# Kernel tuning notes

Measured on AMD Instinct MI355X. Metric: run time of the kernel, lower is better.

## Reference

```python
import jax, jax.numpy as jnp
import numpy as np

N_NODES = 100000
N_EDGES = 300000
NUM_GRAPHS = 2000
IN_DIM = 82
HIDDEN = 256


def _gcn_conv(x, src, dst, dinv, W, b):
    # GCNConv: out = D^-1/2 (A + I) D^-1/2 (x W) + b
    xW = x @ W  # [N, H]
    norm = dinv[src] * dinv[dst]  # [E]
    agg = jax.ops.segment_sum(xW[src] * norm[:, None], dst, num_segments=N_NODES)
    self_loop = xW * (dinv * dinv)[:, None]
    return agg + self_loop + b


def setup_inputs() -> dict:
    key = jax.random.key(0)
    ks = jax.random.split(key, 8)
    x = jax.random.normal(ks[0], (N_NODES, IN_DIM), dtype=jnp.float32)
    edge_index = jax.random.randint(ks[1], (2, N_EDGES), 0, N_NODES, dtype=jnp.int64)
    batch = jnp.sort(jax.random.randint(ks[2], (N_NODES,), 0, NUM_GRAPHS, dtype=jnp.int64))
    W1 = jax.random.normal(ks[3], (IN_DIM, HIDDEN), dtype=jnp.float32) * (1.0 / np.sqrt(IN_DIM))
    W2 = jax.random.normal(ks[4], (HIDDEN, HIDDEN), dtype=jnp.float32) * (1.0 / np.sqrt(HIDDEN))
    W3 = jax.random.normal(ks[5], (HIDDEN, HIDDEN), dtype=jnp.float32) * (1.0 / np.sqrt(HIDDEN))
    b1 = jnp.zeros((HIDDEN,), jnp.float32)
    b2 = jnp.zeros((HIDDEN,), jnp.float32)
    b3 = jnp.zeros((HIDDEN,), jnp.float32)
    return {"x": x, "edge_index": edge_index, "batch": batch, "num_graphs": NUM_GRAPHS,
            "W1": W1, "b1": b1, "W2": W2, "b2": b2, "W3": W3, "b3": b3}


def reference(x, edge_index, batch, num_graphs, W1, b1, W2, b2, W3, b3):
    src, dst = edge_index[0], edge_index[1]
    # symmetric normalization with added self-loops (PyG gcn_norm)
    deg = jax.ops.segment_sum(jnp.ones_like(dst, dtype=x.dtype), dst, num_segments=N_NODES) + 1.0
    dinv = jax.lax.rsqrt(deg)
    h = jax.nn.relu(_gcn_conv(x, src, dst, dinv, W1, b1))
    h = jax.nn.relu(_gcn_conv(h, src, dst, dinv, W2, b2))
    h = jax.nn.relu(_gcn_conv(h, src, dst, dinv, W3, b3))
    return jax.ops.segment_max(h, batch, num_segments=num_graphs)  # [G, H]
```

## Files before the change

### kernel.cpp

```cpp
#include <hip/hip_runtime.h>
#include <cstdint>
#include <cstddef>

#define N_NODES 100000
#define N_EDGES 300000
#define N_GRAPHS 2000
#define HID 256
#define INDIM 82
#define XCPAD 84
#define K1PAD 128
#define N_TILES ((N_NODES + 255) / 256)
#define SCAN_CHUNK 2048
#define NBLK_SCAN ((N_NODES + SCAN_CHUNK - 1) / SCAN_CHUNK)

typedef __bf16 bf16x8 __attribute__((ext_vector_type(8)));
typedef float f32x4 __attribute__((ext_vector_type(4)));

__device__ __forceinline__ unsigned short f2bf(float f) {
    union { __bf16 h; unsigned short u; } v;
    v.h = (__bf16)f;
    return v.u;
}
__device__ __forceinline__ float bf2f(unsigned short s) {
    return __uint_as_float(((unsigned int)s) << 16);
}

__global__ void k_cnt_acc(const int* __restrict__ ei, int* cnt) {
    int e = blockIdx.x * 256 + threadIdx.x;
    if (e < N_EDGES) atomicAdd(&cnt[ei[N_EDGES + e]], 1);
}

__global__ __launch_bounds__(256) void k_scan1(const int* __restrict__ cnt, int* __restrict__ off,
                                               int* __restrict__ partial) {
    __shared__ int sdata[256];
    const int base = blockIdx.x * SCAN_CHUNK;
    const int t = threadIdx.x;
    int v[8];
    int s = 0;
#pragma unroll
    for (int i = 0; i < 8; ++i) {
        int idx = base + t * 8 + i;
        v[i] = (idx < N_NODES) ? cnt[idx] : 0;
        s += v[i];
    }
    sdata[t] = s;
    __syncthreads();
    for (int d = 1; d < 256; d <<= 1) {
        int x = (t >= d) ? sdata[t - d] : 0;
        __syncthreads();
        sdata[t] += x;
        __syncthreads();
    }
    int run = sdata[t] - s;
#pragma unroll
    for (int i = 0; i < 8; ++i) {
        int idx = base + t * 8 + i;
        if (idx < N_NODES) off[idx] = run;
        run += v[i];
    }
    if (t == 255) partial[blockIdx.x] = sdata[255];
}

__global__ void k_scan2(int* partial) {
    if (threadIdx.x == 0 && blockIdx.x == 0) {
        int run = 0;
        for (int i = 0; i < NBLK_SCAN; ++i) {
            int v = partial[i];
            partial[i] = run;
            run += v;
        }
    }
}

__global__ void k_scan3(int* __restrict__ off, const int* __restrict__ partial,
                        int* __restrict__ cur, const int* __restrict__ cnt,
                        float* __restrict__ dinv) {
    int i = blockIdx.x * 256 + threadIdx.x;
    if (i < N_NODES) {
        int o = off[i] + partial[i >> 11];
        off[i] = o;
        cur[i] = o;
        dinv[i] = rsqrtf((float)cnt[i] + 1.0f);
    }
}

__global__ void k_fill(const int* __restrict__ ei, const float* __restrict__ dinv, int* cur,
                       int* __restrict__ csr_src, float* __restrict__ csr_norm) {
    int e = blockIdx.x * 256 + threadIdx.x;
    if (e < N_EDGES) {
        int s = ei[e];
        int d = ei[N_EDGES + e];
        int pos = atomicAdd(&cur[d], 1);
        csr_src[pos] = s;
        csr_norm[pos] = dinv[s] * dinv[d];
    }
}

__device__ __forceinline__ void wconv_body(const float* __restrict__ W,
                                           unsigned short* __restrict__ Wb, int KSRC, int i) {
    int kc = i >> 13;
    int r = i & 8191;
    int nt = r >> 9;
    int r2 = r & 511;
    int lg = r2 >> 7;
    int lr = (r2 >> 3) & 15;
    int j = r2 & 7;
    int k = kc * 32 + lg * 8 + j;
    int n = nt * 16 + lr;
    Wb[i] = (k < KSRC) ? f2bf(W[(size_t)k * HID + n]) : (unsigned short)0;
}

#define PREP_W1 128
#define PREP_W23 256
#define PREP_BND 8
#define PREP_XC ((N_NODES * XCPAD + 255) / 256)
#define PREP_BLOCKS (PREP_W1 + 2 * PREP_W23 + PREP_BND + PREP_XC)

__global__ void k_prep(const float* __restrict__ x, unsigned short* __restrict__ xc,
                       const float* __restrict__ W1, unsigned short* __restrict__ Wb1,
                       const float* __restrict__ W2, unsigned short* __restrict__ Wb2,
                       const float* __restrict__ W3, unsigned short* __restrict__ Wb3,
                       const int* __restrict__ batch, int* __restrict__ gstart) {
    int b = blockIdx.x;
    int t = threadIdx.x;
    if (b < PREP_W1) { wconv_body(W1, Wb1, INDIM, b * 256 + t); return; }
    b -= PREP_W1;
    if (b < PREP_W23) { wconv_body(W2, Wb2, HID, b * 256 + t); return; }
    b -= PREP_W23;
    if (b < PREP_W23) { wconv_body(W3, Wb3, HID, b * 256 + t); return; }
    b -= PREP_W23;
    if (b < PREP_BND) {
        int g = b * 256 + t;
        if (g <= N_GRAPHS) {
            int lo = 0, hi = N_NODES;
            while (lo < hi) {
                int mid = (lo + hi) >> 1;
                if (batch[mid] < g) lo = mid + 1;
                else hi = mid;
            }
            gstart[g] = lo;
        }
        return;
    }
    b -= PREP_BND;
    int i = b * 256 + t;
    if (i < N_NODES * XCPAD) {
        int node = i / XCPAD;
        int k = i - node * XCPAD;
        xc[i] = (k < INDIM) ? f2bf(x[(size_t)node * INDIM + k]) : (unsigned short)0;
    }
}

template <int K>
__global__ __launch_bounds__(512) void k_gemm_mfma(const unsigned short* __restrict__ A,
                                                   const unsigned short* __restrict__ Wb,
                                                   const float* __restrict__ bias,
                                                   unsigned short* __restrict__ Cb) {
    constexpr int NK = K / 32;
    __shared__ __align__(16) unsigned short Wsh[K * HID];

    const int tid = threadIdx.x;
    const int w = tid >> 6;
    const int l = tid & 63;
    const int lr = l & 15;
    const int lg = l >> 4;

#pragma unroll
    for (int i = 0; i < K / 16; ++i) {
        int o = (i * 512 + tid) * 8;
        *reinterpret_cast<uint4*>(&Wsh[o]) = *reinterpret_cast<const uint4*>(Wb + o);
    }
    __syncthreads();

    float bv[16];
#pragma unroll
    for (int nt = 0; nt < 16; ++nt) bv[nt] = bias[nt * 16 + lr];

    for (int t = blockIdx.x; t < N_TILES; t += 256) {
        const int rowbase = t * 256 + w * 32;
        int r0 = rowbase + lr;
        int r1 = rowbase + 16 + lr;
        int r0c = r0 < N_NODES ? r0 : (N_NODES - 1);
        int r1c = r1 < N_NODES ? r1 : (N_NODES - 1);
        const unsigned short* a0p = A + (size_t)r0c * K + lg * 8;
        const unsigned short* a1p = A + (size_t)r1c * K + lg * 8;

        bf16x8 a0[NK], a1[NK];
#pragma unroll
        for (int kc = 0; kc < NK; ++kc) {
            a0[kc] = *reinterpret_cast<const bf16x8*>(a0p + kc * 32);
            a1[kc] = *reinterpret_cast<const bf16x8*>(a1p + kc * 32);
        }

        f32x4 acc0[16] = {};
        f32x4 acc1[16] = {};

#pragma unroll
        for (int kc = 0; kc < NK; ++kc) {
            const unsigned short* bfp = Wsh + kc * 8192 + l * 8;
#pragma unroll
            for (int nt = 0; nt < 16; ++nt) {
                bf16x8 bb = *reinterpret_cast<const bf16x8*>(bfp + nt * 512);
                acc0[nt] = __builtin_amdgcn_mfma_f32_16x16x32_bf16(a0[kc], bb, acc0[nt], 0, 0, 0);
                acc1[nt] = __builtin_amdgcn_mfma_f32_16x16x32_bf16(a1[kc], bb, acc1[nt], 0, 0, 0);
            }
        }

        int gr0 = rowbase + lg * 4;
#pragma unroll
        for (int j = 0; j < 4; ++j) {
            int gr = gr0 + j;
            if (gr < N_NODES) {
                size_t base = (size_t)gr * HID + lr;
#pragma unroll
                for (int nt = 0; nt < 16; ++nt)
                    Cb[base + nt * 16] = f2bf(fmaxf(acc0[nt][j] + bv[nt], 0.0f));
            }
            int gr2 = gr + 16;
            if (gr2 < N_NODES) {
                size_t base = (size_t)gr2 * HID + lr;
#pragma unroll
                for (int nt = 0; nt < 16; ++nt)
                    Cb[base + nt * 16] = f2bf(fmaxf(acc1[nt][j] + bv[nt], 0.0f));
            }
        }
    }
}

__global__ void k_aggregate256(const unsigned short* __restrict__ tb,
                               const float* __restrict__ dinv, const int* __restrict__ off,
                               const int* __restrict__ cnt, const int* __restrict__ csr_src,
                               const float* __restrict__ csr_norm,
                               unsigned short* __restrict__ ob) {
    int node = blockIdx.x * 4 + (threadIdx.x >> 6);
    if (node >= N_NODES) return;
    int lane = threadIdx.x & 63;
    const size_t lo = (size_t)lane * 4;
    int o0 = off[node];
    int n = cnt[node];
    float di = dinv[node];
    float s2 = di * di;
    ushort4 sv = *reinterpret_cast<const ushort4*>(&tb[(size_t)node * HID + lo]);
    float4 acc = {bf2f(sv.x) * s2, bf2f(sv.y) * s2, bf2f(sv.z) * s2, bf2f(sv.w) * s2};

    int j = 0;
    for (; j + 3 < n; j += 4) {
        int s0 = csr_src[o0 + j];
        int s1 = csr_src[o0 + j + 1];
        int s2i = csr_src[o0 + j + 2];
        int s3 = csr_src[o0 + j + 3];
        float n0 = csr_norm[o0 + j];
        float n1 = csr_norm[o0 + j + 1];
        float n2 = csr_norm[o0 + j + 2];
        float n3 = csr_norm[o0 + j + 3];
        ushort4 u0 = *reinterpret_cast<const ushort4*>(&tb[(size_t)s0 * HID + lo]);
        ushort4 u1 = *reinterpret_cast<const ushort4*>(&tb[(size_t)s1 * HID + lo]);
        ushort4 u2 = *reinterpret_cast<const ushort4*>(&tb[(size_t)s2i * HID + lo]);
        ushort4 u3 = *reinterpret_cast<const ushort4*>(&tb[(size_t)s3 * HID + lo]);
        acc.x = fmaf(n0, bf2f(u0.x), acc.x); acc.y = fmaf(n0, bf2f(u0.y), acc.y);
        acc.z = fmaf(n0, bf2f(u0.z), acc.z); acc.w = fmaf(n0, bf2f(u0.w), acc.w);
        acc.x = fmaf(n1, bf2f(u1.x), acc.x); acc.y = fmaf(n1, bf2f(u1.y), acc.y);
        acc.z = fmaf(n1, bf2f(u1.z), acc.z); acc.w = fmaf(n1, bf2f(u1.w), acc.w);
        acc.x = fmaf(n2, bf2f(u2.x), acc.x); acc.y = fmaf(n2, bf2f(u2.y), acc.y);
        acc.z = fmaf(n2, bf2f(u2.z), acc.z); acc.w = fmaf(n2, bf2f(u2.w), acc.w);
        acc.x = fmaf(n3, bf2f(u3.x), acc.x); acc.y = fmaf(n3, bf2f(u3.y), acc.y);
        acc.z = fmaf(n3, bf2f(u3.z), acc.z); acc.w = fmaf(n3, bf2f(u3.w), acc.w);
    }
    int rem = n - j;
    if (rem & 2) {
        int s0 = csr_src[o0 + j];
        int s1 = csr_src[o0 + j + 1];
        float n0 = csr_norm[o0 + j];
        float n1 = csr_norm[o0 + j + 1];
        ushort4 u0 = *reinterpret_cast<const ushort4*>(&tb[(size_t)s0 * HID + lo]);
        ushort4 u1 = *reinterpret_cast<const ushort4*>(&tb[(size_t)s1 * HID + lo]);
        acc.x = fmaf(n0, bf2f(u0.x), acc.x); acc.y = fmaf(n0, bf2f(u0.y), acc.y);
        acc.z = fmaf(n0, bf2f(u0.z), acc.z); acc.w = fmaf(n0, bf2f(u0.w), acc.w);
        acc.x = fmaf(n1, bf2f(u1.x), acc.x); acc.y = fmaf(n1, bf2f(u1.y), acc.y);
        acc.z = fmaf(n1, bf2f(u1.z), acc.z); acc.w = fmaf(n1, bf2f(u1.w), acc.w);
        j += 2;
    }
    if (rem & 1) {
        int s0 = csr_src[o0 + j];
        float n0 = csr_norm[o0 + j];
        ushort4 u0 = *reinterpret_cast<const ushort4*>(&tb[(size_t)s0 * HID + lo]);
        acc.x = fmaf(n0, bf2f(u0.x), acc.x); acc.y = fmaf(n0, bf2f(u0.y), acc.y);
        acc.z = fmaf(n0, bf2f(u0.z), acc.z); acc.w = fmaf(n0, bf2f(u0.w), acc.w);
    }
    ushort4 o;
    o.x = f2bf(acc.x);
    o.y = f2bf(acc.y);
    o.z = f2bf(acc.z);
    o.w = f2bf(acc.w);
    *reinterpret_cast<ushort4*>(&ob[(size_t)node * HID + lo]) = o;
}

__global__ void k_aggx(const unsigned short* __restrict__ xc,
                       const float* __restrict__ dinv, const int* __restrict__ off,
                       const int* __restrict__ cnt, const int* __restrict__ csr_src,
                       const float* __restrict__ csr_norm,
                       unsigned short* __restrict__ ob) {
    int node = blockIdx.x * 4 + (threadIdx.x >> 6);
    if (node >= N_NODES) return;
    int lane = threadIdx.x & 63;
    const bool act = lane < (XCPAD / 2);
    const size_t co = (size_t)lane * 2;
    int o0 = off[node];
    int n = cnt[node];
    float di = dinv[node];
    float s2 = di * di;
    float2 acc = {0.0f, 0.0f};
    if (act) {
        ushort2 sv = *reinterpret_cast<const ushort2*>(&xc[(size_t)node * XCPAD + co]);
        acc.x = bf2f(sv.x) * s2;
        acc.y = bf2f(sv.y) * s2;
    }
    int j = 0;
    for (; j + 3 < n; j += 4) {
        int s0 = csr_src[o0 + j];
        int s1 = csr_src[o0 + j + 1];
        int s2i = csr_src[o0 + j + 2];
        int s3 = csr_src[o0 + j + 3];
        float n0 = csr_norm[o0 + j];
        float n1 = csr_norm[o0 + j + 1];
        float n2 = csr_norm[o0 + j + 2];
        float n3 = csr_norm[o0 + j + 3];
        if (act) {
            ushort2 u0 = *reinterpret_cast<const ushort2*>(&xc[(size_t)s0 * XCPAD + co]);
            ushort2 u1 = *reinterpret_cast<const ushort2*>(&xc[(size_t)s1 * XCPAD + co]);
            ushort2 u2 = *reinterpret_cast<const ushort2*>(&xc[(size_t)s2i * XCPAD + co]);
            ushort2 u3 = *reinterpret_cast<const ushort2*>(&xc[(size_t)s3 * XCPAD + co]);
            acc.x = fmaf(n0, bf2f(u0.x), acc.x); acc.y = fmaf(n0, bf2f(u0.y), acc.y);
            acc.x = fmaf(n1, bf2f(u1.x), acc.x); acc.y = fmaf(n1, bf2f(u1.y), acc.y);
            acc.x = fmaf(n2, bf2f(u2.x), acc.x); acc.y = fmaf(n2, bf2f(u2.y), acc.y);
            acc.x = fmaf(n3, bf2f(u3.x), acc.x); acc.y = fmaf(n3, bf2f(u3.y), acc.y);
        }
    }
    int rem = n - j;
    if (rem & 2) {
        int s0 = csr_src[o0 + j];
        int s1 = csr_src[o0 + j + 1];
        float n0 = csr_norm[o0 + j];
        float n1 = csr_norm[o0 + j + 1];
        if (act) {
            ushort2 u0 = *reinterpret_cast<const ushort2*>(&xc[(size_t)s0 * XCPAD + co]);
            ushort2 u1 = *reinterpret_cast<const ushort2*>(&xc[(size_t)s1 * XCPAD + co]);
            acc.x = fmaf(n0, bf2f(u0.x), acc.x); acc.y = fmaf(n0, bf2f(u0.y), acc.y);
            acc.x = fmaf(n1, bf2f(u1.x), acc.x); acc.y = fmaf(n1, bf2f(u1.y), acc.y);
        }
        j += 2;
    }
    if (rem & 1) {
        int s0 = csr_src[o0 + j];
        float n0 = csr_norm[o0 + j];
        if (act) {
            ushort2 u0 = *reinterpret_cast<const ushort2*>(&xc[(size_t)s0 * XCPAD + co]);
            acc.x = fmaf(n0, bf2f(u0.x), acc.x); acc.y = fmaf(n0, bf2f(u0.y), acc.y);
        }
    }
    ushort2 o;
    o.x = f2bf(acc.x);
    o.y = f2bf(acc.y);
    *reinterpret_cast<ushort2*>(&ob[(size_t)node * K1PAD + co]) = o;
}

__global__ void k_pool2(const unsigned short* __restrict__ hb, const int* __restrict__ gstart,
                        float* __restrict__ out) {
    int g = blockIdx.x;
    int w = threadIdx.x >> 6;
    int lane = threadIdx.x & 63;
    int col = w * 128 + lane * 2;
    int s = gstart[g], e = gstart[g + 1];
    float2 m = {0.0f, 0.0f};
    for (int i = s; i < e; ++i) {
        ushort2 u = *reinterpret_cast<const ushort2*>(&hb[(size_t)i * HID + col]);
        m.x = fmaxf(m.x, bf2f(u.x));
        m.y = fmaxf(m.y, bf2f(u.y));
    }
    *reinterpret_cast<float2*>(&out[(size_t)g * HID + col]) = m;
}

extern "C" void kernel_launch(void* const* d_in, const int* in_sizes, int n_in,
                              void* d_out, int out_size, void* d_ws, size_t ws_size,
                              hipStream_t stream) {
    const float* x = (const float*)d_in[0];
    const int* ei = (const int*)d_in[1];
    const int* batch = (const int*)d_in[2];
    const float* W1 = (const float*)d_in[4];
    const float* b1 = (const float*)d_in[5];
    const float* W2 = (const float*)d_in[6];
    const float* b2 = (const float*)d_in[7];
    const float* W3 = (const float*)d_in[8];
    const float* b3 = (const float*)d_in[9];
    float* out = (float*)d_out;

    char* ws = (char*)d_ws;
    float* dinv = (float*)(ws);
    int* cnt = (int*)(ws + (512 << 10));
    int* off = (int*)(ws + (1024 << 10));
    int* cur = (int*)(ws + (1536 << 10));
    int* part = (int*)(ws + (2048 << 10));
    int* gstart = (int*)(ws + (2048 << 10) + 4096);
    int* csr_src = (int*)(ws + (2176 << 10));
    float* csr_norm = (float*)(ws + (3392 << 10));
    unsigned short* Wb1 = (unsigned short*)(ws + (4608 << 10));
    unsigned short* Wb2 = (unsigned short*)(ws + (4736 << 10));
    unsigned short* Wb3 = (unsigned short*)(ws + (4928 << 10));
    unsigned short* ag1_b = (unsigned short*)(ws + (5120 << 10));
    unsigned short* bufA = (unsigned short*)(ws + (5120 << 10) + 25600000);
    unsigned short* bufB = (unsigned short*)(ws + (5120 << 10) + 76800000);
    unsigned short* x_c = (unsigned short*)(ws + (5120 << 10) + 128000000);

    const int nblk_edges = (N_EDGES + 255) / 256;
    const int nblk_nodes = (N_NODES + 255) / 256;
    const int nblk_rows4 = (N_NODES + 3) / 4;

    hipMemsetAsync(cnt, 0, N_NODES * sizeof(int), stream);
    k_cnt_acc<<<nblk_edges, 256, 0, stream>>>(ei, cnt);
    k_scan1<<<NBLK_SCAN, 256, 0, stream>>>(cnt, off, part);
    k_scan2<<<1, 64, 0, stream>>>(part);
    k_scan3<<<nblk_nodes, 256, 0, stream>>>(off, part, cur, cnt, dinv);
    k_fill<<<nblk_edges, 256, 0, stream>>>(ei, dinv, cur, csr_src, csr_norm);

    k_prep<<<PREP_BLOCKS, 256, 0, stream>>>(x, x_c, W1, Wb1, W2, Wb2, W3, Wb3, batch, gstart);

    k_aggx<<<nblk_rows4, 256, 0, stream>>>(x_c, dinv, off, cnt, csr_src, csr_norm, ag1_b);
    k_gemm_mfma<K1PAD><<<256, 512, 0, stream>>>(ag1_b, Wb1, b1, bufA);

    k_aggregate256<<<nblk_rows4, 256, 0, stream>>>(bufA, dinv, off, cnt, csr_src, csr_norm, bufB);
    k_gemm_mfma<HID><<<256, 512, 0, stream>>>(bufB, Wb2, b2, bufA);

    k_aggregate256<<<nblk_rows4, 256, 0, stream>>>(bufA, dinv, off, cnt, csr_src, csr_norm, bufB);
    k_gemm_mfma<HID><<<256, 512, 0, stream>>>(bufB, Wb3, b3, bufA);

    k_pool2<<<N_GRAPHS, 128, 0, stream>>>(bufA, gstart, out);
}
```

Measured before the change: 257.8 us.

## Fuse neighbor aggregation into MFMA GEMM A-operand loads for layers one and two

Adds a kernel that gathers and normalizes neighbor rows directly while building the MFMA A fragments, removing the separate aggregation kernel and its intermediate buffer round trip for layers 1 and 2. Layer 1 now pads the input to K=96 instead of 128, shrinking the padded GEMM work. Layer 3 keeps the separate aggregate+GEMM path. The fused path performs irregular gathers inside the GEMM loop with one lane group per row, which can hurt latency hiding and occupancy given the large register footprint.

Result: slower. 324.8 us (+26.0%).

```diff
diff --git a/kernel.cpp b/kernel.cpp
--- a/kernel.cpp
+++ b/kernel.cpp
@@ -7,8 +7,7 @@
 #define N_GRAPHS 2000
 #define HID 256
 #define INDIM 82
-#define XCPAD 84
-#define K1PAD 128
+#define K1 96
 #define N_TILES ((N_NODES + 255) / 256)
 #define SCAN_CHUNK 2048
 #define NBLK_SCAN ((N_NODES + SCAN_CHUNK - 1) / SCAN_CHUNK)
@@ -110,10 +109,10 @@
     Wb[i] = (k < KSRC) ? f2bf(W[(size_t)k * HID + n]) : (unsigned short)0;
 }
 
-#define PREP_W1 128
+#define PREP_W1 96
 #define PREP_W23 256
 #define PREP_BND 8
-#define PREP_XC ((N_NODES * XCPAD + 255) / 256)
+#define PREP_XC ((N_NODES * K1 + 255) / 256)
 #define PREP_BLOCKS (PREP_W1 + 2 * PREP_W23 + PREP_BND + PREP_XC)
 
 __global__ void k_prep(const float* __restrict__ x, unsigned short* __restrict__ xc,
@@ -144,10 +143,147 @@
     }
     b -= PREP_BND;
     int i = b * 256 + t;
-    if (i < N_NODES * XCPAD) {
-        int node = i / XCPAD;
-        int k = i - node * XCPAD;
+    if (i < N_NODES * K1) {
+        int node = i / K1;
+        int k = i - node * K1;
         xc[i] = (k < INDIM) ? f2bf(x[(size_t)node * INDIM + k]) : (unsigned short)0;
+    }
+}
+
+template <int K>
+__global__ __launch_bounds__(512) void k_gemm_agg(const unsigned short* __restrict__ A,
+                                                  const unsigned short* __restrict__ Wb,
+                                                  const float* __restrict__ bias,
+                                                  const float* __restrict__ dinv,
+                                                  const int* __restrict__ off,
+                                                  const int* __restrict__ cnt,
+                                                  const int* __restrict__ csr_src,
+                                                  const float* __restrict__ csr_norm,
+                                                  unsigned short* __restrict__ Cb) {
+    constexpr int NK = K / 32;
+    __shared__ __align__(16) unsigned short Wsh[K * HID];
+
+    const int tid = threadIdx.x;
+    const int w = tid >> 6;
+    const int l = tid & 63;
+    const int lr = l & 15;
+    const int lg = l >> 4;
+
+#pragma unroll
+    for (int i = 0; i < K / 16; ++i) {
+        int o = (i * 512 + tid) * 8;
+        *reinterpret_cast<uint4*>(&Wsh[o]) = *reinterpret_cast<const uint4*>(Wb + o);
+    }
+    __syncthreads();
+
+    float bv[16];
+#pragma unroll
+    for (int nt = 0; nt < 16; ++nt) bv[nt] = bias[nt * 16 + lr];
+
+    for (int t = blockIdx.x; t < N_TILES; t += gridDim.x) {
+        const int rowbase = t * 256 + w * 32;
+        int r0 = rowbase + lr;
+        int r1 = rowbase + 16 + lr;
+        int r0c = r0 < N_NODES ? r0 : (N_NODES - 1);
+        int r1c = r1 < N_NODES ? r1 : (N_NODES - 1);
+        const int o00 = off[r0c], n0 = cnt[r0c];
+        const int o01 = off[r1c], n1 = cnt[r1c];
+        float d0 = dinv[r0c], d1 = dinv[r1c];
+        const float s20 = d0 * d0, s21 = d1 * d1;
+
+        f32x4 acc0[16] = {};
+        f32x4 acc1[16] = {};
+
+#pragma unroll
+        for (int kc = 0; kc < NK; ++kc) {
+            const int ko = kc * 32 + lg * 8;
+
+            float ag[8];
+            {
+                bf16x8 sv = *reinterpret_cast<const bf16x8*>(A + (size_t)r0c * K + ko);
+#pragma unroll
+                for (int i = 0; i < 8; ++i) ag[i] = (float)sv[i] * s20;
+                int j = 0;
+                for (; j + 1 < n0; j += 2) {
+                    int sA = csr_src[o00 + j];
+                    int sB = csr_src[o00 + j + 1];
+                    float mA = csr_norm[o00 + j];
+                    float mB = csr_norm[o00 + j + 1];
+                    bf16x8 vA = *reinterpret_cast<const bf16x8*>(A + (size_t)sA * K + ko);
+                    bf16x8 vB = *reinterpret_cast<const bf16x8*>(A + (size_t)sB * K + ko);
+#pragma unroll
+                    for (int i = 0; i < 8; ++i) ag[i] = fmaf(mA, (float)vA[i], ag[i]);
+#pragma unroll
+                    for (int i = 0; i < 8; ++i) ag[i] = fmaf(mB, (float)vB[i], ag[i]);
+                }
+                if (j < n0) {
+                    int sA = csr_src[o00 + j];
+                    float mA = csr_norm[o00 + j];
+                    bf16x8 vA = *reinterpret_cast<const bf16x8*>(A + (size_t)sA * K + ko);
+#pragma unroll
+                    for (int i = 0; i < 8; ++i) ag[i] = fmaf(mA, (float)vA[i], ag[i]);
+                }
+            }
+            bf16x8 a0;
+#pragma unroll
+            for (int i = 0; i < 8; ++i) a0[i] = (__bf16)ag[i];
+
+            {
+                bf16x8 sv = *reinterpret_cast<const bf16x8*>(A + (size_t)r1c * K + ko);
+#pragma unroll
+                for (int i = 0; i < 8; ++i) ag[i] = (float)sv[i] * s21;
+                int j = 0;
+                for (; j + 1 < n1; j += 2) {
+                    int sA = csr_src[o01 + j];
+                    int sB = csr_src[o01 + j + 1];
+                    float mA = csr_norm[o01 + j];
+                    float mB = csr_norm[o01 + j + 1];
+                    bf16x8 vA = *reinterpret_cast<const bf16x8*>(A + (size_t)sA * K + ko);
+                    bf16x8 vB = *reinterpret_cast<const bf16x8*>(A + (size_t)sB * K + ko);
+#pragma unroll
+                    for (int i = 0; i < 8; ++i) ag[i] = fmaf(mA, (float)vA[i], ag[i]);
+#pragma unroll
+                    for (int i = 0; i < 8; ++i) ag[i] = fmaf(mB, (float)vB[i], ag[i]);
+                }
+                if (j < n1) {
+                    int sA = csr_src[o01 + j];
+                    float mA = csr_norm[o01 + j];
+                    bf16x8 vA = *reinterpret_cast<const bf16x8*>(A + (size_t)sA * K + ko);
+#pragma unroll
+                    for (int i = 0; i < 8; ++i) ag[i] = fmaf(mA, (float)vA[i], ag[i]);
+                }
+            }
+            bf16x8 a1;
+#pragma unroll
+            for (int i = 0; i < 8; ++i) a1[i] = (__bf16)ag[i];
+
+            const unsigned short* bfp = Wsh + kc * 8192 + l * 8;
+#pragma unroll
+            for (int nt = 0; nt < 16; ++nt) {
+                bf16x8 bb = *reinterpret_cast<const bf16x8*>(bfp + nt * 512);
+                acc0[nt] = __builtin_amdgcn_mfma_f32_16x16x32_bf16(a0, bb, acc0[nt], 0, 0, 0);
+                acc1[nt] = __builtin_amdgcn_mfma_f32_16x16x32_bf16(a1, bb, acc1[nt], 0, 0, 0);
+            }
+        }
+
+        int gr0 = rowbase + lg * 4;
+#pragma unroll
+        for (int j = 0; j < 4; ++j) {
+            int gr = gr0 + j;
+            if (gr < N_NODES) {
+                size_t base = (size_t)gr * HID + lr;
+#pragma unroll
+                for (int nt = 0; nt < 16; ++nt)
+                    Cb[base + nt * 16] = f2bf(fmaxf(acc0[nt][j] + bv[nt], 0.0f));
+            }
+            int gr2 = gr + 16;
+            if (gr2 < N_NODES) {
+                size_t base = (size_t)gr2 * HID + lr;
+#pragma unroll
+                for (int nt = 0; nt < 16; ++nt)
+                    Cb[base + nt * 16] = f2bf(fmaxf(acc1[nt][j] + bv[nt], 0.0f));
+            }
+        }
     }
 }
 
@@ -176,7 +312,7 @@
 #pragma unroll
     for (int nt = 0; nt < 16; ++nt) bv[nt] = bias[nt * 16 + lr];
 
-    for (int t = blockIdx.x; t < N_TILES; t += 256) {
+    for (int t = blockIdx.x; t < N_TILES; t += gridDim.x) {
         const int rowbase = t * 256 + w * 32;
         int r0 = rowbase + lr;
         int r1 = rowbase + 16 + lr;
@@ -295,75 +431,6 @@
     *reinterpret_cast<ushort4*>(&ob[(size_t)node * HID + lo]) = o;
 }
 
-__global__ void k_aggx(const unsigned short* __restrict__ xc,
-                       const float* __restrict__ dinv, const int* __restrict__ off,
-                       const int* __restrict__ cnt, const int* __restrict__ csr_src,
-                       const float* __restrict__ csr_norm,
-                       unsigned short* __restrict__ ob) {
-    int node = blockIdx.x * 4 + (threadIdx.x >> 6);
-    if (node >= N_NODES) return;
-    int lane = threadIdx.x & 63;
-    const bool act = lane < (XCPAD / 2);
-    const size_t co = (size_t)lane * 2;
-    int o0 = off[node];
-    int n = cnt[node];
-    float di = dinv[node];
-    float s2 = di * di;
-    float2 acc = {0.0f, 0.0f};
-    if (act) {
-        ushort2 sv = *reinterpret_cast<const ushort2*>(&xc[(size_t)node * XCPAD + co]);
-        acc.x = bf2f(sv.x) * s2;
-        acc.y = bf2f(sv.y) * s2;
-    }
-    int j = 0;
-    for (; j + 3 < n; j += 4) {
-        int s0 = csr_src[o0 + j];
-        int s1 = csr_src[o0 + j + 1];
-        int s2i = csr_src[o0 + j + 2];
-        int s3 = csr_src[o0 + j + 3];
-        float n0 = csr_norm[o0 + j];
-        float n1 = csr_norm[o0 + j + 1];
-        float n2 = csr_norm[o0 + j + 2];
-        float n3 = csr_norm[o0 + j + 3];
-        if (act) {
-            ushort2 u0 = *reinterpret_cast<const ushort2*>(&xc[(size_t)s0 * XCPAD + co]);
-            ushort2 u1 = *reinterpret_cast<const ushort2*>(&xc[(size_t)s1 * XCPAD + co]);
-            ushort2 u2 = *reinterpret_cast<const ushort2*>(&xc[(size_t)s2i * XCPAD + co]);
-            ushort2 u3 = *reinterpret_cast<const ushort2*>(&xc[(size_t)s3 * XCPAD + co]);
-            acc.x = fmaf(n0, bf2f(u0.x), acc.x); acc.y = fmaf(n0, bf2f(u0.y), acc.y);
-            acc.x = fmaf(n1, bf2f(u1.x), acc.x); acc.y = fmaf(n1, bf2f(u1.y), acc.y);
-            acc.x = fmaf(n2, bf2f(u2.x), acc.x); acc.y = fmaf(n2, bf2f(u2.y), acc.y);
-            acc.x = fmaf(n3, bf2f(u3.x), acc.x); acc.y = fmaf(n3, bf2f(u3.y), acc.y);
-        }
-    }
-    int rem = n - j;
-    if (rem & 2) {
-        int s0 = csr_src[o0 + j];
-        int s1 = csr_src[o0 + j + 1];
-        float n0 = csr_norm[o0 + j];
-        float n1 = csr_norm[o0 + j + 1];
-        if (act) {
-            ushort2 u0 = *reinterpret_cast<const ushort2*>(&xc[(size_t)s0 * XCPAD + co]);
-            ushort2 u1 = *reinterpret_cast<const ushort2*>(&xc[(size_t)s1 * XCPAD + co]);
-            acc.x = fmaf(n0, bf2f(u0.x), acc.x); acc.y = fmaf(n0, bf2f(u0.y), acc.y);
-            acc.x = fmaf(n1, bf2f(u1.x), acc.x); acc.y = fmaf(n1, bf2f(u1.y), acc.y);
-        }
-        j += 2;
-    }
-    if (rem & 1) {
-        int s0 = csr_src[o0 + j];
-        float n0 = csr_norm[o0 + j];
-        if (act) {
-            ushort2 u0 = *reinterpret_cast<const ushort2*>(&xc[(size_t)s0 * XCPAD + co]);
-            acc.x = fmaf(n0, bf2f(u0.x), acc.x); acc.y = fmaf(n0, bf2f(u0.y), acc.y);
-        }
-    }
-    ushort2 o;
-    o.x = f2bf(acc.x);
-    o.y = f2bf(acc.y);
-    *reinterpret_cast<ushort2*>(&ob[(size_t)node * K1PAD + co]) = o;
-}
-
 __global__ void k_pool2(const unsigned short* __restrict__ hb, const int* __restrict__ gstart,
                         float* __restrict__ out) {
     int g = blockIdx.x;
@@ -406,10 +473,10 @@
     unsigned short* Wb1 = (unsigned short*)(ws + (4608 << 10));
     unsigned short* Wb2 = (unsigned short*)(ws + (4736 << 10));
     unsigned short* Wb3 = (unsigned short*)(ws + (4928 << 10));
-    unsigned short* ag1_b = (unsigned short*)(ws + (5120 << 10));
-    unsigned short* bufA = (unsigned short*)(ws + (5120 << 10) + 25600000);
-    unsigned short* bufB = (unsigned short*)(ws + (5120 << 10) + 76800000);
-    unsigned short* x_c = (unsigned short*)(ws + (5120 << 10) + 128000000);
+    unsigned short* x_c = (unsigned short*)(ws + (5120 << 10));
+    unsigned short* bufA = (unsigned short*)(ws + (5120 << 10) + 19200000);
+    unsigned short* bufB = (unsigned short*)(ws + (5120 << 10) + 70400000);
+    unsigned short* bufC = (unsigned short*)(ws + (5120 << 10) + 121600000);
 
     const int nblk_edges = (N_EDGES + 255) / 256;
     const int nblk_nodes = (N_NODES + 255) / 256;
@@ -424,14 +491,14 @@
 
     k_prep<<<PREP_BLOCKS, 256, 0, stream>>>(x, x_c, W1, Wb1, W2, Wb2, W3, Wb3, batch, gstart);
 
-    k_aggx<<<nblk_rows4, 256, 0, stream>>>(x_c, dinv, off, cnt, csr_src, csr_norm, ag1_b);
-    k_gemm_mfma<K1PAD><<<256, 512, 0, stream>>>(ag1_b, Wb1, b1, bufA);
-
-    k_aggregate256<<<nblk_rows4, 256, 0, stream>>>(bufA, dinv, off, cnt, csr_src, csr_norm, bufB);
-    k_gemm_mfma<HID><<<256, 512, 0, stream>>>(bufB, Wb2, b2, bufA);
-
-    k_aggregate256<<<nblk_rows4, 256, 0, stream>>>(bufA, dinv, off, cnt, csr_src, csr_norm, bufB);
-    k_gemm_mfma<HID><<<256, 512, 0, stream>>>(bufB, Wb3, b3, bufA);
+    k_gemm_agg<K1><<<N_TILES, 512, 0, stream>>>(x_c, Wb1, b1, dinv, off, cnt, csr_src,
+                                                csr_norm, bufA);
+
+    k_gemm_agg<HID><<<256, 512, 0, stream>>>(bufA, Wb2, b2, dinv, off, cnt, csr_src,
+                                             csr_norm, bufB);
+
+    k_aggregate256<<<nblk_rows4, 256, 0, stream>>>(bufB, dinv, off, cnt, csr_src, csr_norm, bufC);
+    k_gemm_mfma<HID><<<256, 512, 0, stream>>>(bufC, Wb3, b3, bufA);
 
     k_pool2<<<N_GRAPHS, 128, 0, stream>>>(bufA, gstart, out);
 }
```

## Split GEMM columns across two blocks per tile and shrink layer-1 K to 96

Applied to the files above, without the earlier changes.

The GEMM kernel drops its persistent grid-stride loop over row tiles. It now launches two blocks per 256-row tile, and each block covers half of the 256 output columns. This halves the shared-memory weight footprint and the accumulator registers per block, so more blocks can be resident and more parallelism is exposed. Separately, the layer-1 input is padded to 96 instead of the earlier 84/128 mix: the aggregated features are stored at width 96 and the first GEMM runs with K=96, which removes wasted MFMA work and memory traffic. In exchange, each tile's A rows are now loaded twice (once per column half), and every block reloads its half of the weights.

Result: slower. 279.2 us (+8.3%).

```diff
diff --git a/kernel.cpp b/kernel.cpp
--- a/kernel.cpp
+++ b/kernel.cpp
@@ -7,8 +7,7 @@
 #define N_GRAPHS 2000
 #define HID 256
 #define INDIM 82
-#define XCPAD 84
-#define K1PAD 128
+#define K1 96
 #define N_TILES ((N_NODES + 255) / 256)
 #define SCAN_CHUNK 2048
 #define NBLK_SCAN ((N_NODES + SCAN_CHUNK - 1) / SCAN_CHUNK)
@@ -110,10 +109,10 @@
     Wb[i] = (k < KSRC) ? f2bf(W[(size_t)k * HID + n]) : (unsigned short)0;
 }
 
-#define PREP_W1 128
+#define PREP_W1 96
 #define PREP_W23 256
 #define PREP_BND 8
-#define PREP_XC ((N_NODES * XCPAD + 255) / 256)
+#define PREP_XC ((N_NODES * K1 + 255) / 256)
 #define PREP_BLOCKS (PREP_W1 + 2 * PREP_W23 + PREP_BND + PREP_XC)
 
 __global__ void k_prep(const float* __restrict__ x, unsigned short* __restrict__ xc,
@@ -144,9 +143,9 @@
     }
     b -= PREP_BND;
     int i = b * 256 + t;
-    if (i < N_NODES * XCPAD) {
-        int node = i / XCPAD;
-        int k = i - node * XCPAD;
+    if (i < N_NODES * K1) {
+        int node = i / K1;
+        int k = i - node * K1;
         xc[i] = (k < INDIM) ? f2bf(x[(size_t)node * INDIM + k]) : (unsigned short)0;
     }
 }
@@ -157,72 +156,72 @@
                                                    const float* __restrict__ bias,
                                                    unsigned short* __restrict__ Cb) {
     constexpr int NK = K / 32;
-    __shared__ __align__(16) unsigned short Wsh[K * HID];
+    __shared__ __align__(16) unsigned short Wsh[K * 128];
 
     const int tid = threadIdx.x;
     const int w = tid >> 6;
     const int l = tid & 63;
     const int lr = l & 15;
     const int lg = l >> 4;
-
-#pragma unroll
-    for (int i = 0; i < K / 16; ++i) {
-        int o = (i * 512 + tid) * 8;
-        *reinterpret_cast<uint4*>(&Wsh[o]) = *reinterpret_cast<const uint4*>(Wb + o);
+    const int t = blockIdx.x >> 1;
+    const int ch = blockIdx.x & 1;
+
+#pragma unroll
+    for (int i = 0; i < NK; ++i) {
+        *reinterpret_cast<uint4*>(&Wsh[i * 4096 + tid * 8]) =
+            *reinterpret_cast<const uint4*>(Wb + i * 8192 + ch * 4096 + tid * 8);
     }
     __syncthreads();
 
-    float bv[16];
-#pragma unroll
-    for (int nt = 0; nt < 16; ++nt) bv[nt] = bias[nt * 16 + lr];
-
-    for (int t = blockIdx.x; t < N_TILES; t += 256) {
-        const int rowbase = t * 256 + w * 32;
-        int r0 = rowbase + lr;
-        int r1 = rowbase + 16 + lr;
-        int r0c = r0 < N_NODES ? r0 : (N_NODES - 1);
-        int r1c = r1 < N_NODES ? r1 : (N_NODES - 1);
-        const unsigned short* a0p = A + (size_t)r0c * K + lg * 8;
-        const unsigned short* a1p = A + (size_t)r1c * K + lg * 8;
-
-        bf16x8 a0[NK], a1[NK];
-#pragma unroll
-        for (int kc = 0; kc < NK; ++kc) {
-            a0[kc] = *reinterpret_cast<const bf16x8*>(a0p + kc * 32);
-            a1[kc] = *reinterpret_cast<const bf16x8*>(a1p + kc * 32);
-        }
-
-        f32x4 acc0[16] = {};
-        f32x4 acc1[16] = {};
-
-#pragma unroll
-        for (int kc = 0; kc < NK; ++kc) {
-            const unsigned short* bfp = Wsh + kc * 8192 + l * 8;
-#pragma unroll
-            for (int nt = 0; nt < 16; ++nt) {
-                bf16x8 bb = *reinterpret_cast<const bf16x8*>(bfp + nt * 512);
-                acc0[nt] = __builtin_amdgcn_mfma_f32_16x16x32_bf16(a0[kc], bb, acc0[nt], 0, 0, 0);
-                acc1[nt] = __builtin_amdgcn_mfma_f32_16x16x32_bf16(a1[kc], bb, acc1[nt], 0, 0, 0);
-            }
-        }
-
-        int gr0 = rowbase + lg * 4;
-#pragma unroll
-        for (int j = 0; j < 4; ++j) {
-            int gr = gr0 + j;
-            if (gr < N_NODES) {
-                size_t base = (size_t)gr * HID + lr;
-#pragma unroll
-                for (int nt = 0; nt < 16; ++nt)
-                    Cb[base + nt * 16] = f2bf(fmaxf(acc0[nt][j] + bv[nt], 0.0f));
-            }
-            int gr2 = gr + 16;
-            if (gr2 < N_NODES) {
-                size_t base = (size_t)gr2 * HID + lr;
-#pragma unroll
-                for (int nt = 0; nt < 16; ++nt)
-                    Cb[base + nt * 16] = f2bf(fmaxf(acc1[nt][j] + bv[nt], 0.0f));
-            }
+    float bv[8];
+#pragma unroll
+    for (int nt = 0; nt < 8; ++nt) bv[nt] = bias[ch * 128 + nt * 16 + lr];
+
+    const int rowbase = t * 256 + w * 32;
+    int r0 = rowbase + lr;
+    int r1 = rowbase + 16 + lr;
+    int r0c = r0 < N_NODES ? r0 : (N_NODES - 1);
+    int r1c = r1 < N_NODES ? r1 : (N_NODES - 1);
+    const unsigned short* a0p = A + (size_t)r0c * K + lg * 8;
+    const unsigned short* a1p = A + (size_t)r1c * K + lg * 8;
+
+    bf16x8 a0[NK], a1[NK];
+#pragma unroll
+    for (int kc = 0; kc < NK; ++kc) {
+        a0[kc] = *reinterpret_cast<const bf16x8*>(a0p + kc * 32);
+        a1[kc] = *reinterpret_cast<const bf16x8*>(a1p + kc * 32);
+    }
+
+    f32x4 acc0[8] = {};
+    f32x4 acc1[8] = {};
+
+#pragma unroll
+    for (int kc = 0; kc < NK; ++kc) {
+        const unsigned short* bfp = Wsh + kc * 4096 + l * 8;
+#pragma unroll
+        for (int nt = 0; nt < 8; ++nt) {
+            bf16x8 bb = *reinterpret_cast<const bf16x8*>(bfp + nt * 512);
+            acc0[nt] = __builtin_amdgcn_mfma_f32_16x16x32_bf16(a0[kc], bb, acc0[nt], 0, 0, 0);
+            acc1[nt] = __builtin_amdgcn_mfma_f32_16x16x32_bf16(a1[kc], bb, acc1[nt], 0, 0, 0);
+        }
+    }
+
+    int gr0 = rowbase + lg * 4;
+#pragma unroll
+    for (int j = 0; j < 4; ++j) {
+        int gr = gr0 + j;
+        if (gr < N_NODES) {
+            size_t base = (size_t)gr * HID + ch * 128 + lr;
+#pragma unroll
+            for (int nt = 0; nt < 8; ++nt)
+                Cb[base + nt * 16] = f2bf(fmaxf(acc0[nt][j] + bv[nt], 0.0f));
+        }
+        int gr2 = gr + 16;
+        if (gr2 < N_NODES) {
+            size_t base = (size_t)gr2 * HID + ch * 128 + lr;
+#pragma unroll
+            for (int nt = 0; nt < 8; ++nt)
+                Cb[base + nt * 16] = f2bf(fmaxf(acc1[nt][j] + bv[nt], 0.0f));
         }
     }
 }
@@ -295,15 +294,15 @@
     *reinterpret_cast<ushort4*>(&ob[(size_t)node * HID + lo]) = o;
 }
 
-__global__ void k_aggx(const unsigned short* __restrict__ xc,
-                       const float* __restrict__ dinv, const int* __restrict__ off,
-                       const int* __restrict__ cnt, const int* __restrict__ csr_src,
-                       const float* __restrict__ csr_norm,
-                       unsigned short* __restrict__ ob) {
+__global__ void k_aggx96(const unsigned short* __restrict__ xc,
+                         const float* __restrict__ dinv, const int* __restrict__ off,
+                         const int* __restrict__ cnt, const int* __restrict__ csr_src,
+                         const float* __restrict__ csr_norm,
+                         unsigned short* __restrict__ ob) {
     int node = blockIdx.x * 4 + (threadIdx.x >> 6);
     if (node >= N_NODES) return;
     int lane = threadIdx.x & 63;
-    const bool act = lane < (XCPAD / 2);
+    const bool act = lane < (K1 / 2);
     const size_t co = (size_t)lane * 2;
     int o0 = off[node];
     int n = cnt[node];
@@ -311,7 +310,7 @@
     float s2 = di * di;
     float2 acc = {0.0f, 0.0f};
     if (act) {
-        ushort2 sv = *reinterpret_cast<const ushort2*>(&xc[(size_t)node * XCPAD + co]);
+        ushort2 sv = *reinterpret_cast<const ushort2*>(&xc[(size_t)node * K1 + co]);
         acc.x = bf2f(sv.x) * s2;
         acc.y = bf2f(sv.y) * s2;
     }
@@ -326,10 +325,10 @@
         float n2 = csr_norm[o0 + j + 2];
         float n3 = csr_norm[o0 + j + 3];
         if (act) {
-            ushort2 u0 = *reinterpret_cast<const ushort2*>(&xc[(size_t)s0 * XCPAD + co]);
-            ushort2 u1 = *reinterpret_cast<const ushort2*>(&xc[(size_t)s1 * XCPAD + co]);
-            ushort2 u2 = *reinterpret_cast<const ushort2*>(&xc[(size_t)s2i * XCPAD + co]);
-            ushort2 u3 = *reinterpret_cast<const ushort2*>(&xc[(size_t)s3 * XCPAD + co]);
+            ushort2 u0 = *reinterpret_cast<const ushort2*>(&xc[(size_t)s0 * K1 + co]);
+            ushort2 u1 = *reinterpret_cast<const ushort2*>(&xc[(size_t)s1 * K1 + co]);
+            ushort2 u2 = *reinterpret_cast<const ushort2*>(&xc[(size_t)s2i * K1 + co]);
+            ushort2 u3 = *reinterpret_cast<const ushort2*>(&xc[(size_t)s3 * K1 + co]);
             acc.x = fmaf(n0, bf2f(u0.x), acc.x); acc.y = fmaf(n0, bf2f(u0.y), acc.y);
             acc.x = fmaf(n1, bf2f(u1.x), acc.x); acc.y = fmaf(n1, bf2f(u1.y), acc.y);
             acc.x = fmaf(n2, bf2f(u2.x), acc.x); acc.y = fmaf(n2, bf2f(u2.y), acc.y);
@@ -343,8 +342,8 @@
         float n0 = csr_norm[o0 + j];
         float n1 = csr_norm[o0 + j + 1];
         if (act) {
-            ushort2 u0 = *reinterpret_cast<const ushort2*>(&xc[(size_t)s0 * XCPAD + co]);
-            ushort2 u1 = *reinterpret_cast<const ushort2*>(&xc[(size_t)s1 * XCPAD + co]);
+            ushort2 u0 = *reinterpret_cast<const ushort2*>(&xc[(size_t)s0 * K1 + co]);
+            ushort2 u1 = *reinterpret_cast<const ushort2*>(&xc[(size_t)s1 * K1 + co]);
             acc.x = fmaf(n0, bf2f(u0.x), acc.x); acc.y = fmaf(n0, bf2f(u0.y), acc.y);
             acc.x = fmaf(n1, bf2f(u1.x), acc.x); acc.y = fmaf(n1, bf2f(u1.y), acc.y);
         }
@@ -354,14 +353,16 @@
         int s0 = csr_src[o0 + j];
         float n0 = csr_norm[o0 + j];
         if (act) {
-            ushort2 u0 = *reinterpret_cast<const ushort2*>(&xc[(size_t)s0 * XCPAD + co]);
+            ushort2 u0 = *reinterpret_cast<const ushort2*>(&xc[(size_t)s0 * K1 + co]);
             acc.x = fmaf(n0, bf2f(u0.x), acc.x); acc.y = fmaf(n0, bf2f(u0.y), acc.y);
         }
     }
-    ushort2 o;
-    o.x = f2bf(acc.x);
-    o.y = f2bf(acc.y);
-    *reinterpret_cast<ushort2*>(&ob[(size_t)node * K1PAD + co]) = o;
+    if (act) {
+        ushort2 o;
+        o.x = f2bf(acc.x);
+        o.y = f2bf(acc.y);
+        *reinterpret_cast<ushort2*>(&ob[(size_t)node * K1 + co]) = o;
+    }
 }
 
 __global__ void k_pool2(const unsigned short* __restrict__ hb, const int* __restrict__ gstart,
@@ -406,10 +407,10 @@
     unsigned short* Wb1 = (unsigned short*)(ws + (4608 << 10));
     unsigned short* Wb2 = (unsigned short*)(ws + (4736 << 10));
     unsigned short* Wb3 = (unsigned short*)(ws + (4928 << 10));
-    unsigned short* ag1_b = (unsigned short*)(ws + (5120 << 10));
-    unsigned short* bufA = (unsigned short*)(ws + (5120 << 10) + 25600000);
-    unsigned short* bufB = (unsigned short*)(ws + (5120 << 10) + 76800000);
-    unsigned short* x_c = (unsigned short*)(ws + (5120 << 10) + 128000000);
+    unsigned short* x_c = (unsigned short*)(ws + (5120 << 10));
+    unsigned short* ag1 = (unsigned short*)(ws + (5120 << 10) + 19200000);
+    unsigned short* bufA = (unsigned short*)(ws + (5120 << 10) + 38400000);
+    unsigned short* bufB = (unsigned short*)(ws + (5120 << 10) + 89600000);
 
     const int nblk_edges = (N_EDGES + 255) / 256;
     const int nblk_nodes = (N_NODES + 255) / 256;
@@ -424,14 +425,14 @@
 
     k_prep<<<PREP_BLOCKS, 256, 0, stream>>>(x, x_c, W1, Wb1, W2, Wb2, W3, Wb3, batch, gstart);
 
-    k_aggx<<<nblk_rows4, 256, 0, stream>>>(x_c, dinv, off, cnt, csr_src, csr_norm, ag1_b);
-    k_gemm_mfma<K1PAD><<<256, 512, 0, stream>>>(ag1_b, Wb1, b1, bufA);
+    k_aggx96<<<nblk_rows4, 256, 0, stream>>>(x_c, dinv, off, cnt, csr_src, csr_norm, ag1);
+    k_gemm_mfma<K1><<<N_TILES * 2, 512, 0, stream>>>(ag1, Wb1, b1, bufA);
 
     k_aggregate256<<<nblk_rows4, 256, 0, stream>>>(bufA, dinv, off, cnt, csr_src, csr_norm, bufB);
-    k_gemm_mfma<HID><<<256, 512, 0, stream>>>(bufB, Wb2, b2, bufA);
+    k_gemm_mfma<HID><<<N_TILES * 2, 512, 0, stream>>>(bufB, Wb2, b2, bufA);
 
     k_aggregate256<<<nblk_rows4, 256, 0, stream>>>(bufA, dinv, off, cnt, csr_src, csr_norm, bufB);
-    k_gemm_mfma<HID><<<256, 512, 0, stream>>>(bufB, Wb3, b3, bufA);
+    k_gemm_mfma<HID><<<N_TILES * 2, 512, 0, stream>>>(bufB, Wb3, b3, bufA);
 
     k_pool2<<<N_GRAPHS, 128, 0, stream>>>(bufA, gstart, out);
 }
```

## Split GEMM tiles across column halves and prefetch next tile's A fragments

Applied to the files above, without the earlier changes.

Each block now handles a 128-row tile, and each pair of waves splits the 256 output columns into two halves. This halves the accumulator registers per wave so occupancy can rise. For K=256 the next tile's A fragments are register-prefetched while the current tile computes, hiding global load latency. The K=128 GEMM launches 512 blocks with a min-waves-per-EU hint of 4 and no prefetch. The prefetch doubles the fragment registers and may cause spills or limit occupancy.

Result: slower. 463.1 us (+79.7%).

```diff
diff --git a/kernel.cpp b/kernel.cpp
--- a/kernel.cpp
+++ b/kernel.cpp
@@ -9,7 +9,7 @@
 #define INDIM 82
 #define XCPAD 84
 #define K1PAD 128
-#define N_TILES ((N_NODES + 255) / 256)
+#define NT128 ((N_NODES + 127) / 128)
 #define SCAN_CHUNK 2048
 #define NBLK_SCAN ((N_NODES + SCAN_CHUNK - 1) / SCAN_CHUNK)
 
@@ -151,11 +151,26 @@
     }
 }
 
-template <int K>
-__global__ __launch_bounds__(512) void k_gemm_mfma(const unsigned short* __restrict__ A,
-                                                   const unsigned short* __restrict__ Wb,
-                                                   const float* __restrict__ bias,
-                                                   unsigned short* __restrict__ Cb) {
+#define LOAD_FRAGS(T, F0, F1)                                              \
+    do {                                                                   \
+        int rb_ = (T) * 128 + wr * 32;                                     \
+        int rr0_ = rb_ + lr;                                               \
+        if (rr0_ >= N_NODES) rr0_ = N_NODES - 1;                           \
+        int rr1_ = rb_ + 16 + lr;                                          \
+        if (rr1_ >= N_NODES) rr1_ = N_NODES - 1;                           \
+        const unsigned short* p0_ = A + (size_t)rr0_ * K + lg * 8;         \
+        const unsigned short* p1_ = A + (size_t)rr1_ * K + lg * 8;         \
+        _Pragma("unroll") for (int kc_ = 0; kc_ < NK; ++kc_) {             \
+            F0[kc_] = *reinterpret_cast<const bf16x8*>(p0_ + kc_ * 32);    \
+            F1[kc_] = *reinterpret_cast<const bf16x8*>(p1_ + kc_ * 32);    \
+        }                                                                  \
+    } while (0)
+
+template <int K, bool PF, int MINW>
+__global__ __launch_bounds__(512, MINW) void k_gemm_mfma(const unsigned short* __restrict__ A,
+                                                         const unsigned short* __restrict__ Wb,
+                                                         const float* __restrict__ bias,
+                                                         unsigned short* __restrict__ Cb) {
     constexpr int NK = K / 32;
     __shared__ __align__(16) unsigned short Wsh[K * HID];
 
@@ -164,6 +179,8 @@
     const int l = tid & 63;
     const int lr = l & 15;
     const int lg = l >> 4;
+    const int wr = w >> 1;
+    const int ch = w & 1;
 
 #pragma unroll
     for (int i = 0; i < K / 16; ++i) {
@@ -172,57 +189,62 @@
     }
     __syncthreads();
 
-    float bv[16];
-#pragma unroll
-    for (int nt = 0; nt < 16; ++nt) bv[nt] = bias[nt * 16 + lr];
-
-    for (int t = blockIdx.x; t < N_TILES; t += 256) {
-        const int rowbase = t * 256 + w * 32;
-        int r0 = rowbase + lr;
-        int r1 = rowbase + 16 + lr;
-        int r0c = r0 < N_NODES ? r0 : (N_NODES - 1);
-        int r1c = r1 < N_NODES ? r1 : (N_NODES - 1);
-        const unsigned short* a0p = A + (size_t)r0c * K + lg * 8;
-        const unsigned short* a1p = A + (size_t)r1c * K + lg * 8;
-
-        bf16x8 a0[NK], a1[NK];
+    float bv[8];
+#pragma unroll
+    for (int nt = 0; nt < 8; ++nt) bv[nt] = bias[ch * 128 + nt * 16 + lr];
+
+    bf16x8 A0[NK], A1[NK], B0[NK], B1[NK];
+    int t = blockIdx.x;
+    if (t < NT128) LOAD_FRAGS(t, A0, A1);
+
+    for (; t < NT128; t += gridDim.x) {
+        if (PF) {
+            int tn = t + gridDim.x;
+            int tnc = tn < NT128 ? tn : t;
+            LOAD_FRAGS(tnc, B0, B1);
+        }
+
+        f32x4 acc0[8] = {};
+        f32x4 acc1[8] = {};
 #pragma unroll
         for (int kc = 0; kc < NK; ++kc) {
-            a0[kc] = *reinterpret_cast<const bf16x8*>(a0p + kc * 32);
-            a1[kc] = *reinterpret_cast<const bf16x8*>(a1p + kc * 32);
-        }
-
-        f32x4 acc0[16] = {};
-        f32x4 acc1[16] = {};
-
-#pragma unroll
-        for (int kc = 0; kc < NK; ++kc) {
-            const unsigned short* bfp = Wsh + kc * 8192 + l * 8;
-#pragma unroll
-            for (int nt = 0; nt < 16; ++nt) {
+            const unsigned short* bfp = Wsh + kc * 8192 + ch * 4096 + l * 8;
+#pragma unroll
+            for (int nt = 0; nt < 8; ++nt) {
                 bf16x8 bb = *reinterpret_cast<const bf16x8*>(bfp + nt * 512);
-                acc0[nt] = __builtin_amdgcn_mfma_f32_16x16x32_bf16(a0[kc], bb, acc0[nt], 0, 0, 0);
-                acc1[nt] = __builtin_amdgcn_mfma_f32_16x16x32_bf16(a1[kc], bb, acc1[nt], 0, 0, 0);
+                acc0[nt] = __builtin_amdgcn_mfma_f32_16x16x32_bf16(A0[kc], bb, acc0[nt], 0, 0, 0);
+                acc1[nt] = __builtin_amdgcn_mfma_f32_16x16x32_bf16(A1[kc], bb, acc1[nt], 0, 0, 0);
             }
         }
 
-        int gr0 = rowbase + lg * 4;
+        int gr0 = t * 128 + wr * 32 + lg * 4;
 #pragma unroll
         for (int j = 0; j < 4; ++j) {
             int gr = gr0 + j;
             if (gr < N_NODES) {
-                size_t base = (size_t)gr * HID + lr;
-#pragma unroll
-                for (int nt = 0; nt < 16; ++nt)
+                size_t base = (size_t)gr * HID + ch * 128 + lr;
+#pragma unroll
+                for (int nt = 0; nt < 8; ++nt)
                     Cb[base + nt * 16] = f2bf(fmaxf(acc0[nt][j] + bv[nt], 0.0f));
             }
             int gr2 = gr + 16;
             if (gr2 < N_NODES) {
-                size_t base = (size_t)gr2 * HID + lr;
-#pragma unroll
-                for (int nt = 0; nt < 16; ++nt)
+                size_t base = (size_t)gr2 * HID + ch * 128 + lr;
+#pragma unroll
+                for (int nt = 0; nt < 8; ++nt)
                     Cb[base + nt * 16] = f2bf(fmaxf(acc1[nt][j] + bv[nt], 0.0f));
             }
+        }
+
+        if (PF) {
+#pragma unroll
+            for (int kc = 0; kc < NK; ++kc) {
+                A0[kc] = B0[kc];
+                A1[kc] = B1[kc];
+            }
+        } else {
+            int tn = t + gridDim.x;
+            if (tn < NT128) LOAD_FRAGS(tn, A0, A1);
         }
     }
 }
@@ -425,13 +447,13 @@
     k_prep<<<PREP_BLOCKS, 256, 0, stream>>>(x, x_c, W1, Wb1, W2, Wb2, W3, Wb3, batch, gstart);
 
     k_aggx<<<nblk_rows4, 256, 0, stream>>>(x_c, dinv, off, cnt, csr_src, csr_norm, ag1_b);
-    k_gemm_mfma<K1PAD><<<256, 512, 0, stream>>>(ag1_b, Wb1, b1, bufA);
+    k_gemm_mfma<K1PAD, false, 4><<<512, 512, 0, stream>>>(ag1_b, Wb1, b1, bufA);
 
     k_aggregate256<<<nblk_rows4, 256, 0, stream>>>(bufA, dinv, off, cnt, csr_src, csr_norm, bufB);
-    k_gemm_mfma<HID><<<256, 512, 0, stream>>>(bufB, Wb2, b2, bufA);
+    k_gemm_mfma<HID, true, 2><<<256, 512, 0, stream>>>(bufB, Wb2, b2, bufA);
 
     k_aggregate256<<<nblk_rows4, 256, 0, stream>>>(bufA, dinv, off, cnt, csr_src, csr_norm, bufB);
-    k_gemm_mfma<HID><<<256, 512, 0, stream>>>(bufB, Wb3, b3, bufA);
+    k_gemm_mfma<HID, true, 2><<<256, 512, 0, stream>>>(bufB, Wb3, b3, bufA);
 
     k_pool2<<<N_GRAPHS, 128, 0, stream>>>(bufA, gstart, out);
 }
```
